# Kernel optimization log

Measured on AMD Instinct MI355X. Metric: run time of the kernel, lower is better.

## Reference

```python
import jax, jax.numpy as jnp
import numpy as np

B, T, V, D, L, FFM = 2, 2048, 50257, 1024, 8, 2


def setup_inputs() -> dict:
    key = jax.random.key(0)
    ks = jax.random.split(key, 10)
    s = 0.02
    return {
        "input_ids": jax.random.randint(ks[0], (B, T), 0, V),
        "embed": jax.random.normal(ks[1], (V, D), jnp.float32) * s,
        "norm1_w": jnp.ones((L, D), jnp.float32),
        "norm2_w": jnp.ones((L, D), jnp.float32),
        "a_diag": jax.random.uniform(ks[2], (L, D), jnp.float32, 0.5, 0.99),
        "W_in": jax.random.normal(ks[3], (L, D, D), jnp.float32) * s,
        "b_in": jnp.zeros((L, D), jnp.float32),
        "W_out": jax.random.normal(ks[4], (L, D, D), jnp.float32) * s,
        "ff_w1": jax.random.normal(ks[5], (L, D, FFM * D), jnp.float32) * s,
        "ff_b1": jnp.zeros((L, FFM * D), jnp.float32),
        "ff_w2": jax.random.normal(ks[6], (L, FFM * D, D), jnp.float32) * s,
        "ff_b2": jnp.zeros((L, D), jnp.float32),
        "final_norm_w": jnp.ones((D,), jnp.float32),
        "lm_head_w": jax.random.normal(ks[7], (V, D), jnp.float32) * s,
    }


def rmsnorm(x, w, eps=1e-6):
    return x * jax.lax.rsqrt(jnp.mean(x * x, axis=-1, keepdims=True) + eps) * w


def chaos_core(x, a, Win, bin_, Wout):
    pre = jnp.einsum('btd,de->bte', x, Win) + bin_  # precompute input drive (parallel)

    def step(s, p):
        s = jnp.tanh(a * s + p)
        return s, s

    s0 = jnp.zeros((x.shape[0], x.shape[-1]), x.dtype)
    _, hs = jax.lax.scan(step, s0, jnp.swapaxes(pre, 0, 1))  # (T, B, D)
    hs = jnp.swapaxes(hs, 0, 1)  # (B, T, D)
    return jnp.einsum('btd,de->bte', hs, Wout)


def reference(input_ids, embed, norm1_w, norm2_w, a_diag, W_in, b_in, W_out,
              ff_w1, ff_b1, ff_w2, ff_b2, final_norm_w, lm_head_w):
    x = embed[input_ids]  # (B, T, D)
    for i in range(L):
        # input_norm -> core -> residual
        x = x + chaos_core(rmsnorm(x, norm1_w[i]), a_diag[i], W_in[i], b_in[i], W_out[i])
        # ff_norm -> FeedForward (Linear -> SiLU -> Linear) -> residual
        h = rmsnorm(x, norm2_w[i])
        h = jax.nn.silu(jnp.einsum('btd,df->btf', h, ff_w1[i]) + ff_b1[i])
        x = x + jnp.einsum('btf,fd->btd', h, ff_w2[i]) + ff_b2[i]
    x = rmsnorm(x, final_norm_w)
    return jnp.einsum('btd,vd->btv', x, lm_head_w)  # logits (B, T, V)
```

## Files before the change

### kernel.cpp

```cpp
#include <hip/hip_runtime.h>

typedef unsigned short u16;
typedef __bf16 bf16x8 __attribute__((ext_vector_type(8)));
typedef float f32x4 __attribute__((ext_vector_type(4)));
typedef unsigned short u16x4 __attribute__((ext_vector_type(4)));

__device__ __forceinline__ u16 f2bf(float f) {
  union { float f; unsigned int u; } v; v.f = f;
  return (u16)((v.u + 0x7FFFu + ((v.u >> 16) & 1u)) >> 16);
}

__device__ __forceinline__ void gload16(const void* g, void* l) {
  __builtin_amdgcn_global_load_lds(
      (const __attribute__((address_space(1))) unsigned int*)g,
      (__attribute__((address_space(3))) unsigned int*)l, 16, 0, 0);
}

__global__ void transpose_cast_kernel(const float* __restrict__ W, u16* __restrict__ WT,
                                      int R, int C) {
  __shared__ float tile[32][33];
  const int tx = threadIdx.x, ty = threadIdx.y;
  const size_t zoff = (size_t)blockIdx.z * R * C;
  const int c0 = blockIdx.x * 32, r0 = blockIdx.y * 32;
#pragma unroll
  for (int k = 0; k < 32; k += 8)
    tile[ty + k][tx] = W[zoff + (size_t)(r0 + ty + k) * C + (c0 + tx)];
  __syncthreads();
#pragma unroll
  for (int k = 0; k < 32; k += 8)
    WT[zoff + (size_t)(c0 + ty + k) * R + (r0 + tx)] = f2bf(tile[tx][ty + k]);
}

__global__ void lm_cast_kernel(const float* __restrict__ lm, u16* __restrict__ out) {
  const int row = blockIdx.x;
  const int t = threadIdx.x;
  u16x4 o = {0, 0, 0, 0};
  if (row < 50257) {
    float4 v = *(const float4*)(lm + (size_t)row * 1024 + t * 4);
    o.x = f2bf(v.x); o.y = f2bf(v.y); o.z = f2bf(v.z); o.w = f2bf(v.w);
  }
  *(u16x4*)(out + (size_t)row * 1024 + t * 4) = o;
}

__global__ void embed_kernel(const int* __restrict__ ids, const float* __restrict__ embed,
                             float* __restrict__ x) {
  const int row = blockIdx.x;
  const int id = ids[row];
  const int t = threadIdx.x;
  *(float4*)(x + (size_t)row * 1024 + t * 4) =
      *(const float4*)(embed + (size_t)id * 1024 + t * 4);
}

__global__ void rmsnorm_kernel(const float* __restrict__ x, const float* __restrict__ w,
                               u16* __restrict__ out) {
  const int row = blockIdx.x, tid = threadIdx.x;
  const float* xr = x + (size_t)row * 1024;
  float4 v = *(const float4*)(xr + tid * 4);
  float ss = v.x * v.x + v.y * v.y + v.z * v.z + v.w * v.w;
#pragma unroll
  for (int off = 32; off; off >>= 1) ss += __shfl_xor(ss, off);
  __shared__ float red[4];
  if ((tid & 63) == 0) red[tid >> 6] = ss;
  __syncthreads();
  const float tot = red[0] + red[1] + red[2] + red[3];
  const float r = rsqrtf(tot * (1.0f / 1024.0f) + 1e-6f);
  float4 wv = *(const float4*)(w + tid * 4);
  u16x4 o;
  o.x = f2bf(v.x * r * wv.x); o.y = f2bf(v.y * r * wv.y);
  o.z = f2bf(v.z * r * wv.z); o.w = f2bf(v.w * r * wv.w);
  *(u16x4*)(out + (size_t)row * 1024 + tid * 4) = o;
}

__device__ __forceinline__ void sload(const float* __restrict__ p, int tb,
                                      float A2b, float (&buf)[8]) {
#pragma unroll
  for (int j = 0; j < 8; j++)
    buf[j] = fmaf(p[(size_t)(tb + j) * 1024], 2.8853900817779268f, A2b);
}

__device__ __forceinline__ void scomp(float (&buf)[8], float m2A2, float& r,
                                      u16* __restrict__ o, int tb) {
#pragma unroll
  for (int j = 0; j < 8; j++) {
    float z = fmaf(m2A2, r, buf[j]);
    float e = __builtin_amdgcn_exp2f(z);
    r = __builtin_amdgcn_rcpf(1.0f + e);
    o[(size_t)(tb + j) * 1024] = f2bf(fmaf(-2.0f, r, 1.0f));
  }
}

__global__ __launch_bounds__(256) void scan_kernel(const float* __restrict__ pre,
                                                   const float* __restrict__ a_diag,
                                                   const float* __restrict__ b_in,
                                                   u16* __restrict__ hs) {
  const int T = 2048;
  const int idx = blockIdx.x * 256 + threadIdx.x;
  const int b = idx >> 10, d = idx & 1023;
  const float* p = pre + (size_t)b * T * 1024 + d;
  u16* o = hs + (size_t)b * T * 1024 + d;
  const float A2 = a_diag[d] * 2.8853900817779268f;
  const float A2b = fmaf(2.8853900817779268f, b_in[d], A2);
  const float m2A2 = -2.0f * A2;
  float r = 0.5f;
  float b0[8], b1[8], b2[8], b3[8];
  sload(p, 0, A2b, b0); sload(p, 8, A2b, b1);
  sload(p, 16, A2b, b2); sload(p, 24, A2b, b3);
  for (int t0 = 0; t0 < T; t0 += 32) {
    scomp(b0, m2A2, r, o, t0);
    if (t0 + 32 < T) sload(p, t0 + 32, A2b, b0);
    scomp(b1, m2A2, r, o, t0 + 8);
    if (t0 + 32 < T) sload(p, t0 + 40, A2b, b1);
    scomp(b2, m2A2, r, o, t0 + 16);
    if (t0 + 32 < T) sload(p, t0 + 48, A2b, b2);
    scomp(b3, m2A2, r, o, t0 + 24);
    if (t0 + 32 < T) sload(p, t0 + 56, A2b, b3);
  }
}

template <int EPI>
__global__ __launch_bounds__(256) void gemmL(
    const u16* __restrict__ A, int lda, const u16* __restrict__ Bw, int ldb,
    const float* __restrict__ bias, float* Cf, u16* __restrict__ Cb,
    int ldc, int K) {
  __shared__ char lds[49152];
  const int tid = threadIdx.x;
  const int lane = tid & 63;
  const int wc = tid >> 6;
  const int tm = blockIdx.y * 64, tn = blockIdx.x * 128;
  const int lr = lane & 15;
  const int sb0 = ((lane >> 4) ^ (lane & 7)) << 4;

  const int srow = tid >> 3;
  const int sxs = ((tid & 7) ^ (srow & 7)) << 4;
  const char* pA = (const char*)A + (size_t)(tm + srow) * lda * 2 + sxs;
  const char* pB = (const char*)Bw + (size_t)(tn + srow) * ldb * 2 + sxs;
  const size_t a32 = (size_t)lda * 64;
  const size_t b32 = (size_t)ldb * 64;

#define STGL(kt, bufo)                                \
  {                                                   \
    char* d = lds + (bufo) + tid * 16;                \
    const size_t kb = (size_t)(kt) << 7;              \
    gload16(pA + kb, d);                              \
    gload16(pA + a32 + kb, d + 4096);                 \
    gload16(pB + kb, d + 8192);                       \
    gload16(pB + b32 + kb, d + 12288);                \
    gload16(pB + 2 * b32 + kb, d + 16384);            \
    gload16(pB + 3 * b32 + kb, d + 20480);            \
  }

  f32x4 acc[4][2] = {};
  const int nkt = K >> 6;

  STGL(0, 0);
  int cur = 0;
  for (int kt = 0; kt < nkt; ++kt) {
    if (kt + 1 < nkt) {
      STGL(kt + 1, (cur ^ 1) * 24576);
      asm volatile("s_waitcnt vmcnt(6)" ::: "memory");
    } else {
      asm volatile("s_waitcnt vmcnt(0)" ::: "memory");
    }
    __builtin_amdgcn_s_barrier();
    const char* base = lds + cur * 24576;
    bf16x8 aF[4][2], bF[2][2];
#pragma unroll
    for (int m = 0; m < 4; m++)
#pragma unroll
      for (int ks = 0; ks < 2; ks++)
        aF[m][ks] =
            *(const bf16x8*)(base + (m * 16 + lr) * 128 + (sb0 ^ (ks << 6)));
#pragma unroll
    for (int n = 0; n < 2; n++)
#pragma unroll
      for (int ks = 0; ks < 2; ks++)
        bF[n][ks] = *(const bf16x8*)(base + 8192 +
                                     (wc * 32 + n * 16 + lr) * 128 +
                                     (sb0 ^ (ks << 6)));
#pragma unroll
    for (int ks = 0; ks < 2; ks++)
#pragma unroll
      for (int m = 0; m < 4; m++)
#pragma unroll
        for (int n = 0; n < 2; n++)
          acc[m][n] = __builtin_amdgcn_mfma_f32_16x16x32_bf16(
              aF[m][ks], bF[n][ks], acc[m][n], 0, 0, 0);
    __builtin_amdgcn_s_barrier();
    cur ^= 1;
  }
#undef STGL

  const int crow = tm + ((lane >> 4) << 2);
  const int ccol = tn + wc * 32 + lr;
#pragma unroll
  for (int m = 0; m < 4; m++) {
#pragma unroll
    for (int n = 0; n < 2; n++) {
      const int cg = ccol + n * 16;
      float bb = 0.0f;
      if (EPI == 2 || EPI == 3) bb = bias[cg];
#pragma unroll
      for (int j = 0; j < 4; j++) {
        const size_t off = (size_t)(crow + m * 16 + j) * ldc + cg;
        const float v = acc[m][n][j] + bb;
        if (EPI == 0) {
          Cf[off] = v;
        } else if (EPI == 1) {
          Cf[off] += v;
        } else if (EPI == 2) {
          const float sg = __builtin_amdgcn_rcpf(
              1.0f + __builtin_amdgcn_exp2f(-1.4426950408889634f * v));
          Cb[off] = f2bf(v * sg);
        } else {
          Cf[off] += v;
        }
      }
    }
  }
}

__global__ __launch_bounds__(512, 2) void gemm_lm8(
    const u16* __restrict__ A, const u16* __restrict__ Bw,
    float* __restrict__ C, int Nreal) {
  __shared__ char lds[131072];
  const int tid = threadIdx.x;
  const int lane = tid & 63;
  const int wid = tid >> 6;
  const int wr = wid >> 2;
  const int wc = wid & 3;
  const int bid = blockIdx.x;
  const int tm = (((bid & 7) << 1) + ((bid >> 3) & 1)) << 8;
  const int tn = (bid >> 4) << 8;

  const int srow = tid >> 3;
  const int sxor = ((tid & 7) ^ (srow & 7)) << 4;
  const char* pAs = (const char*)A + ((size_t)(tm + srow) << 11) + sxor;
  const char* pBs = (const char*)Bw + ((size_t)(tn + srow) << 11) + sxor;

#define STG(p, h, kt, ro)                                      \
  {                                                            \
    char* d = lds + (ro) + tid * 16;                           \
    const char* s = (p) + ((size_t)(h) << 18) + ((kt) << 7);   \
    gload16(s, d);                                             \
    gload16(s + (64ull << 11), d + 8192);                      \
  }

  const int lr = lane & 15;
  const int sb0 = (((lane >> 4) ^ (lane & 7)) << 4);
  const int sb[2] = {sb0, sb0 ^ 64};
  const int aB = wr * 16384 + lr * 128;
  const int bB = 32768 + (wc >> 1) * 16384 + ((wc & 1) * 64 + lr) * 128;

  bf16x8 aR[4][2], bR[2][2][2];
  f32x4 acc[8][4] = {};

#define LDA_Q(bufo, mq)                                                         \
  _Pragma("unroll") for (int m_ = 0; m_ < 4; m_++)                              \
  _Pragma("unroll") for (int k_ = 0; k_ < 2; k_++)                              \
      aR[m_][k_] = *(const bf16x8*)(lds + (bufo) + aB + (mq)*8192 + m_*2048 + sb[k_]);

#define LDB_Q(bufo, nq)                                                         \
  _Pragma("unroll") for (int n_ = 0; n_ < 2; n_++)                              \
  _Pragma("unroll") for (int k_ = 0; k_ < 2; k_++)                              \
      bR[nq][n_][k_] = *(const bf16x8*)(lds + (bufo) + bB + (nq)*4096 + n_*2048 + sb[k_]);

#define MFMA_Q(mq, nq)                                                          \
  __builtin_amdgcn_s_setprio(1);                                                \
  _Pragma("unroll") for (int m_ = 0; m_ < 4; m_++)                              \
  _Pragma("unroll") for (int n_ = 0; n_ < 2; n_++)                              \
  _Pragma("unroll") for (int k_ = 0; k_ < 2; k_++)                              \
      acc[(mq)*4 + m_][(nq)*2 + n_] = __builtin_amdgcn_mfma_f32_16x16x32_bf16(  \
          aR[m_][k_], bR[nq][n_][k_], acc[(mq)*4 + m_][(nq)*2 + n_], 0, 0, 0);  \
  __builtin_amdgcn_s_setprio(0);

#define BAR() __builtin_amdgcn_s_barrier()
#define LGKM0() asm volatile("s_waitcnt lgkmcnt(0)" ::: "memory")

  STG(pAs, 0, 0, 0);
  STG(pAs, 1, 0, 16384);
  STG(pBs, 0, 0, 32768);
  STG(pBs, 1, 0, 49152);
  STG(pBs, 0, 1, 65536 + 32768);
  STG(pBs, 1, 1, 65536 + 49152);
  asm volatile("s_waitcnt vmcnt(4)" ::: "memory");
  BAR();

  for (int it = 0; it < 8; ++it) {
    const int t1 = 2 * it + 1, t2 = 2 * it + 2, t3 = 2 * it + 3;
    const bool st = (it < 7);
    LDA_Q(0, 0); LDB_Q(0, 0);
    STG(pAs, 0, t1, 65536);
    BAR(); LGKM0(); MFMA_Q(0, 0); BAR();
    LDB_Q(0, 1);
    STG(pAs, 1, t1, 65536 + 16384);
    BAR(); LGKM0(); MFMA_Q(0, 1); BAR();
    LDA_Q(0, 1);
    if (st) STG(pBs, 0, t2, 32768);
    BAR(); LGKM0(); MFMA_Q(1, 0); BAR();
    if (st) STG(pBs, 1, t2, 49152);
    BAR(); LGKM0(); MFMA_Q(1, 1);
    if (st) { asm volatile("s_waitcnt vmcnt(4)" ::: "memory"); }
    else    { asm volatile("s_waitcnt vmcnt(0)" ::: "memory"); }
    BAR();
    LDA_Q(65536, 0); LDB_Q(65536, 0);
    if (st) STG(pAs, 0, t2, 0);
    BAR(); LGKM0(); MFMA_Q(0, 0); BAR();
    LDB_Q(65536, 1);
    if (st) STG(pAs, 1, t2, 16384);
    BAR(); LGKM0(); MFMA_Q(0, 1); BAR();
    LDA_Q(65536, 1);
    if (st) STG(pBs, 0, t3, 65536 + 32768);
    BAR(); LGKM0(); MFMA_Q(1, 0); BAR();
    if (st) STG(pBs, 1, t3, 65536 + 49152);
    BAR(); LGKM0(); MFMA_Q(1, 1);
    if (st) { asm volatile("s_waitcnt vmcnt(4)" ::: "memory"); }
    else    { asm volatile("s_waitcnt vmcnt(0)" ::: "memory"); }
    BAR();
  }
#undef STG
#undef LDA_Q
#undef LDB_Q
#undef MFMA_Q
#undef BAR
#undef LGKM0

  const int crow = tm + wr * 128 + ((lane >> 4) << 2);
  const int ccol = tn + wc * 64 + lr;
#pragma unroll
  for (int M_ = 0; M_ < 8; M_++) {
    const int r = crow + (M_ >> 2) * 64 + (M_ & 3) * 16;
#pragma unroll
    for (int N_ = 0; N_ < 4; N_++) {
      const int cg = ccol + (N_ >> 1) * 32 + (N_ & 1) * 16;
      if (cg < Nreal) {
#pragma unroll
        for (int j = 0; j < 4; j++)
          __builtin_nontemporal_store(acc[M_][N_][j],
                                      &C[(size_t)(r + j) * Nreal + cg]);
      }
    }
  }
}

extern "C" void kernel_launch(void* const* d_in, const int* in_sizes, int n_in,
                              void* d_out, int out_size, void* d_ws, size_t ws_size,
                              hipStream_t stream) {
  const int D = 1024, V = 50257, L = 8;
  const int M = 4096;
  const int Vpad = 50432;
  const size_t MD = (size_t)M * D;

  const int* ids = (const int*)d_in[0];
  const float* embedw = (const float*)d_in[1];
  const float* norm1_w = (const float*)d_in[2];
  const float* norm2_w = (const float*)d_in[3];
  const float* a_diag = (const float*)d_in[4];
  const float* W_in = (const float*)d_in[5];
  const float* b_in = (const float*)d_in[6];
  const float* W_out = (const float*)d_in[7];
  const float* ff_w1 = (const float*)d_in[8];
  const float* ff_b1 = (const float*)d_in[9];
  const float* ff_w2 = (const float*)d_in[10];
  const float* ff_b2 = (const float*)d_in[11];
  const float* final_norm_w = (const float*)d_in[12];
  const float* lm_head_w = (const float*)d_in[13];

  char* w = (char*)d_ws;
  float* x = (float*)w;   w += MD * 4;
  u16* h = (u16*)w;       w += MD * 2;
  float* pre = (float*)w; w += MD * 4;
  u16* hs = (u16*)w;      w += MD * 2;
  u16* hff = (u16*)w;     w += MD * 2 * 2;
  u16* WinT = (u16*)w;    w += (size_t)L * D * D * 2;
  u16* WoutT = (u16*)w;   w += (size_t)L * D * D * 2;
  u16* ffw1T = (u16*)w;   w += (size_t)L * 2 * D * D * 2;
  u16* ffw2T = (u16*)w;   w += (size_t)L * 2 * D * D * 2;
  u16* lmpad = (u16*)w;   w += (size_t)Vpad * D * 2;

  lm_cast_kernel<<<Vpad, 256, 0, stream>>>(lm_head_w, lmpad);
  transpose_cast_kernel<<<dim3(32, 32, L), dim3(32, 8), 0, stream>>>(W_in, WinT, D, D);
  transpose_cast_kernel<<<dim3(64, 32, L), dim3(32, 8), 0, stream>>>(ff_w1, ffw1T, D, 2 * D);
  transpose_cast_kernel<<<dim3(32, 32, L), dim3(32, 8), 0, stream>>>(W_out, WoutT, D, D);
  transpose_cast_kernel<<<dim3(32, 64, L), dim3(32, 8), 0, stream>>>(ff_w2, ffw2T, 2 * D, D);

  embed_kernel<<<M, 256, 0, stream>>>(ids, embedw, x);

  for (int l = 0; l < L; l++) {
    rmsnorm_kernel<<<M, 256, 0, stream>>>(x, norm1_w + (size_t)l * D, h);
    gemmL<0><<<dim3(8, 64), 256, 0, stream>>>(
        h, D, WinT + (size_t)l * D * D, D, nullptr, pre, nullptr, D, D);
    scan_kernel<<<8, 256, 0, stream>>>(pre, a_diag + (size_t)l * D,
                                       b_in + (size_t)l * D, hs);
    gemmL<1><<<dim3(8, 64), 256, 0, stream>>>(
        hs, D, WoutT + (size_t)l * D * D, D, nullptr, x, nullptr, D, D);
    rmsnorm_kernel<<<M, 256, 0, stream>>>(x, norm2_w + (size_t)l * D, h);
    gemmL<2><<<dim3(16, 64), 256, 0, stream>>>(
        h, D, ffw1T + (size_t)l * 2 * D * D, D, ff_b1 + (size_t)l * 2 * D,
        nullptr, hff, 2 * D, D);
    gemmL<3><<<dim3(8, 64), 256, 0, stream>>>(
        hff, 2 * D, ffw2T + (size_t)l * 2 * D * D, 2 * D,
        ff_b2 + (size_t)l * D, x, nullptr, D, 2 * D);
  }

  rmsnorm_kernel<<<M, 256, 0, stream>>>(x, final_norm_w, h);
  gemm_lm8<<<dim3(8 * 394), 512, 0, stream>>>(h, lmpad, (float*)d_out, V);
}
```

Baseline: 3.027 ms.

## Fuse RMSNorm into GEMM prologue and fold norm weights into transposed weights

```diff
diff --git a/kernel.cpp b/kernel.cpp
--- a/kernel.cpp
+++ b/kernel.cpp
@@ -4,6 +4,7 @@
 typedef __bf16 bf16x8 __attribute__((ext_vector_type(8)));
 typedef float f32x4 __attribute__((ext_vector_type(4)));
 typedef unsigned short u16x4 __attribute__((ext_vector_type(4)));
+typedef unsigned short u16x8 __attribute__((ext_vector_type(8)));
 
 __device__ __forceinline__ u16 f2bf(float f) {
   union { float f; unsigned int u; } v; v.f = f;
@@ -16,19 +17,47 @@
       (__attribute__((address_space(3))) unsigned int*)l, 16, 0, 0);
 }
 
-__global__ void transpose_cast_kernel(const float* __restrict__ W, u16* __restrict__ WT,
-                                      int R, int C) {
+__global__ void prep_weights(const float* __restrict__ Win,
+                             const float* __restrict__ Wout,
+                             const float* __restrict__ ffw1,
+                             const float* __restrict__ ffw2,
+                             const float* __restrict__ n1w,
+                             const float* __restrict__ n2w,
+                             u16* __restrict__ WinT, u16* __restrict__ WoutT,
+                             u16* __restrict__ f1T, u16* __restrict__ f2T) {
   __shared__ float tile[32][33];
+  const int tk = blockIdx.x;
+  const float* src; u16* dst; const float* wm = nullptr;
+  int R, C, tr, tc;
+  if (tk < 8192) {
+    const int l = tk >> 10, rem = tk & 1023;
+    R = 1024; C = 1024; tr = rem >> 5; tc = rem & 31;
+    src = Win + (size_t)l * 1048576; dst = WinT + (size_t)l * 1048576;
+    wm = n1w + l * 1024;
+  } else if (tk < 16384) {
+    const int q = tk - 8192, l = q >> 10, rem = q & 1023;
+    R = 1024; C = 1024; tr = rem >> 5; tc = rem & 31;
+    src = Wout + (size_t)l * 1048576; dst = WoutT + (size_t)l * 1048576;
+  } else if (tk < 32768) {
+    const int q = tk - 16384, l = q >> 11, rem = q & 2047;
+    R = 1024; C = 2048; tr = rem >> 6; tc = rem & 63;
+    src = ffw1 + (size_t)l * 2097152; dst = f1T + (size_t)l * 2097152;
+    wm = n2w + l * 1024;
+  } else {
+    const int q = tk - 32768, l = q >> 11, rem = q & 2047;
+    R = 2048; C = 1024; tr = rem >> 5; tc = rem & 31;
+    src = ffw2 + (size_t)l * 2097152; dst = f2T + (size_t)l * 2097152;
+  }
   const int tx = threadIdx.x, ty = threadIdx.y;
-  const size_t zoff = (size_t)blockIdx.z * R * C;
-  const int c0 = blockIdx.x * 32, r0 = blockIdx.y * 32;
+  const int c0 = tc * 32, r0 = tr * 32;
 #pragma unroll
   for (int k = 0; k < 32; k += 8)
-    tile[ty + k][tx] = W[zoff + (size_t)(r0 + ty + k) * C + (c0 + tx)];
+    tile[ty + k][tx] = src[(size_t)(r0 + ty + k) * C + (c0 + tx)];
   __syncthreads();
+  const float wv = wm ? wm[r0 + tx] : 1.0f;
 #pragma unroll
   for (int k = 0; k < 32; k += 8)
-    WT[zoff + (size_t)(c0 + ty + k) * R + (r0 + tx)] = f2bf(tile[tx][ty + k]);
+    dst[(size_t)(c0 + ty + k) * R + (r0 + tx)] = f2bf(tile[tx][ty + k] * wv);
 }
 
 __global__ void lm_cast_kernel(const float* __restrict__ lm, u16* __restrict__ out) {
@@ -120,8 +149,7 @@
 template <int EPI>
 __global__ __launch_bounds__(256) void gemmL(
     const u16* __restrict__ A, int lda, const u16* __restrict__ Bw, int ldb,
-    const float* __restrict__ bias, float* Cf, u16* __restrict__ Cb,
-    int ldc, int K) {
+    const float* __restrict__ bias, float* Cf, int ldc, int K) {
   __shared__ char lds[49152];
   const int tid = threadIdx.x;
   const int lane = tid & 63;
@@ -197,22 +225,149 @@
 #pragma unroll
     for (int n = 0; n < 2; n++) {
       const int cg = ccol + n * 16;
-      float bb = 0.0f;
-      if (EPI == 2 || EPI == 3) bb = bias[cg];
+      const float bb = (EPI == 3) ? bias[cg] : 0.0f;
+#pragma unroll
+      for (int j = 0; j < 4; j++) {
+        const size_t off = (size_t)(crow + m * 16 + j) * ldc + cg;
+        Cf[off] += acc[m][n][j] + bb;
+      }
+    }
+  }
+}
+
+template <int EPI>
+__global__ __launch_bounds__(256) void gemmLF(
+    const float* __restrict__ X, const u16* __restrict__ Bw, int ldb,
+    const float* __restrict__ bias, float* __restrict__ Cf,
+    u16* __restrict__ Cb, int ldc) {
+  __shared__ char lds[50432];
+  float* red = (float*)(lds + 49152);
+  float* rinvs = (float*)(lds + 50176);
+  const int tid = threadIdx.x;
+  const int lane = tid & 63;
+  const int wc = tid >> 6;
+  const int tm = blockIdx.y * 64, tn = blockIdx.x * 128;
+  const int lr = lane & 15;
+  const int sb0 = ((lane >> 4) ^ (lane & 7)) << 4;
+
+  {
+    const float* xr = X + (size_t)(tm + (tid >> 2)) * 1024 + (tid & 3) * 256;
+    float ss = 0.f;
+#pragma unroll 8
+    for (int j = 0; j < 64; j++) {
+      float4 v = *(const float4*)(xr + j * 4);
+      ss += v.x * v.x + v.y * v.y + v.z * v.z + v.w * v.w;
+    }
+    red[tid] = ss;
+  }
+  __syncthreads();
+  if (tid < 64)
+    rinvs[tid] = rsqrtf((red[tid * 4] + red[tid * 4 + 1] + red[tid * 4 + 2] +
+                         red[tid * 4 + 3]) * (1.0f / 1024.0f) + 1e-6f);
+  __syncthreads();
+  const float rv = rinvs[tid >> 2];
+
+  const int srow = tid >> 3;
+  const int sxs = ((tid & 7) ^ (srow & 7)) << 4;
+  const char* pB = (const char*)Bw + (size_t)(tn + srow) * ldb * 2 + sxs;
+  const size_t b32 = (size_t)ldb * 64;
+  const int arow = tid >> 2;
+  const float* xa = X + (size_t)(tm + arow) * 1024 + (tid & 3) * 16;
+  char* const da = lds + arow * 128;
+  const int as0 = (((tid & 3) * 2) ^ (arow & 7)) << 4;
+  const int as1 = (((tid & 3) * 2 + 1) ^ (arow & 7)) << 4;
+
+#define STB(kt, bufo)                                            \
+  {                                                              \
+    char* d = lds + (bufo) + 8192 + tid * 16;                    \
+    const size_t kb = (size_t)(kt) << 7;                         \
+    gload16(pB + kb, d);                                         \
+    gload16(pB + b32 + kb, d + 4096);                            \
+    gload16(pB + 2 * b32 + kb, d + 8192);                        \
+    gload16(pB + 3 * b32 + kb, d + 12288);                       \
+  }
+#define CVT8(o_, v0_, v1_)                                       \
+  o_[0] = f2bf(v0_.x * rv); o_[1] = f2bf(v0_.y * rv);            \
+  o_[2] = f2bf(v0_.z * rv); o_[3] = f2bf(v0_.w * rv);            \
+  o_[4] = f2bf(v1_.x * rv); o_[5] = f2bf(v1_.y * rv);            \
+  o_[6] = f2bf(v1_.z * rv); o_[7] = f2bf(v1_.w * rv);
+
+  f32x4 acc[4][2] = {};
+
+  {
+    const float* s0 = xa;
+    float4 v0 = *(const float4*)(s0), v1 = *(const float4*)(s0 + 4);
+    float4 v2 = *(const float4*)(s0 + 8), v3 = *(const float4*)(s0 + 12);
+    u16x8 o0, o1;
+    CVT8(o0, v0, v1); CVT8(o1, v2, v3);
+    *(u16x8*)(da + as0) = o0; *(u16x8*)(da + as1) = o1;
+    STB(0, 0);
+  }
+  __syncthreads();
+
+  int cur = 0;
+  for (int kt = 0; kt < 16; ++kt) {
+    const int nb = (cur ^ 1) * 24576;
+    float4 v0, v1, v2, v3;
+    if (kt < 15) {
+      const float* s_ = xa + (kt + 1) * 64;
+      v0 = *(const float4*)(s_); v1 = *(const float4*)(s_ + 4);
+      v2 = *(const float4*)(s_ + 8); v3 = *(const float4*)(s_ + 12);
+      STB(kt + 1, nb);
+    }
+    const char* base = lds + cur * 24576;
+    bf16x8 aF[4][2], bF[2][2];
+#pragma unroll
+    for (int m = 0; m < 4; m++)
+#pragma unroll
+      for (int ks = 0; ks < 2; ks++)
+        aF[m][ks] =
+            *(const bf16x8*)(base + (m * 16 + lr) * 128 + (sb0 ^ (ks << 6)));
+#pragma unroll
+    for (int n = 0; n < 2; n++)
+#pragma unroll
+      for (int ks = 0; ks < 2; ks++)
+        bF[n][ks] = *(const bf16x8*)(base + 8192 +
+                                     (wc * 32 + n * 16 + lr) * 128 +
+                                     (sb0 ^ (ks << 6)));
+#pragma unroll
+    for (int ks = 0; ks < 2; ks++)
+#pragma unroll
+      for (int m = 0; m < 4; m++)
+#pragma unroll
+        for (int n = 0; n < 2; n++)
+          acc[m][n] = __builtin_amdgcn_mfma_f32_16x16x32_bf16(
+              aF[m][ks], bF[n][ks], acc[m][n], 0, 0, 0);
+    if (kt < 15) {
+      u16x8 o0, o1;
+      CVT8(o0, v0, v1); CVT8(o1, v2, v3);
+      *(u16x8*)(lds + nb + (da - lds) + as0) = o0;
+      *(u16x8*)(lds + nb + (da - lds) + as1) = o1;
+    }
+    __syncthreads();
+    cur ^= 1;
+  }
+#undef STB
+#undef CVT8
+
+  const int crow = tm + ((lane >> 4) << 2);
+  const int ccol = tn + wc * 32 + lr;
+#pragma unroll
+  for (int m = 0; m < 4; m++) {
+#pragma unroll
+    for (int n = 0; n < 2; n++) {
+      const int cg = ccol + n * 16;
+      const float bb = (EPI == 2) ? bias[cg] : 0.0f;
 #pragma unroll
       for (int j = 0; j < 4; j++) {
         const size_t off = (size_t)(crow + m * 16 + j) * ldc + cg;
         const float v = acc[m][n][j] + bb;
         if (EPI == 0) {
           Cf[off] = v;
-        } else if (EPI == 1) {
-          Cf[off] += v;
-        } else if (EPI == 2) {
+        } else {
           const float sg = __builtin_amdgcn_rcpf(
               1.0f + __builtin_amdgcn_exp2f(-1.4426950408889634f * v));
           Cb[off] = f2bf(v * sg);
-        } else {
-          Cf[off] += v;
         }
       }
     }
@@ -335,8 +490,7 @@
       if (cg < Nreal) {
 #pragma unroll
         for (int j = 0; j < 4; j++)
-          __builtin_nontemporal_store(acc[M_][N_][j],
-                                      &C[(size_t)(r + j) * Nreal + cg]);
+          C[(size_t)(r + j) * Nreal + cg] = acc[M_][N_][j];
       }
     }
   }
@@ -377,29 +531,24 @@
   u16* ffw2T = (u16*)w;   w += (size_t)L * 2 * D * D * 2;
   u16* lmpad = (u16*)w;   w += (size_t)Vpad * D * 2;
 
+  prep_weights<<<49152, dim3(32, 8), 0, stream>>>(
+      W_in, W_out, ff_w1, ff_w2, norm1_w, norm2_w, WinT, WoutT, ffw1T, ffw2T);
   lm_cast_kernel<<<Vpad, 256, 0, stream>>>(lm_head_w, lmpad);
-  transpose_cast_kernel<<<dim3(32, 32, L), dim3(32, 8), 0, stream>>>(W_in, WinT, D, D);
-  transpose_cast_kernel<<<dim3(64, 32, L), dim3(32, 8), 0, stream>>>(ff_w1, ffw1T, D, 2 * D);
-  transpose_cast_kernel<<<dim3(32, 32, L), dim3(32, 8), 0, stream>>>(W_out, WoutT, D, D);
-  transpose_cast_kernel<<<dim3(32, 64, L), dim3(32, 8), 0, stream>>>(ff_w2, ffw2T, 2 * D, D);
-
   embed_kernel<<<M, 256, 0, stream>>>(ids, embedw, x);
 
   for (int l = 0; l < L; l++) {
-    rmsnorm_kernel<<<M, 256, 0, stream>>>(x, norm1_w + (size_t)l * D, h);
-    gemmL<0><<<dim3(8, 64), 256, 0, stream>>>(
-        h, D, WinT + (size_t)l * D * D, D, nullptr, pre, nullptr, D, D);
+    gemmLF<0><<<dim3(8, 64), 256, 0, stream>>>(
+        x, WinT + (size_t)l * D * D, D, nullptr, pre, nullptr, D);
     scan_kernel<<<8, 256, 0, stream>>>(pre, a_diag + (size_t)l * D,
                                        b_in + (size_t)l * D, hs);
     gemmL<1><<<dim3(8, 64), 256, 0, stream>>>(
-        hs, D, WoutT + (size_t)l * D * D, D, nullptr, x, nullptr, D, D);
-    rmsnorm_kernel<<<M, 256, 0, stream>>>(x, norm2_w + (size_t)l * D, h);
-    gemmL<2><<<dim3(16, 64), 256, 0, stream>>>(
-        h, D, ffw1T + (size_t)l * 2 * D * D, D, ff_b1 + (size_t)l * 2 * D,
-        nullptr, hff, 2 * D, D);
+        hs, D, WoutT + (size_t)l * D * D, D, nullptr, x, D, D);
+    gemmLF<2><<<dim3(16, 64), 256, 0, stream>>>(
+        x, ffw1T + (size_t)l * 2 * D * D, D, ff_b1 + (size_t)l * 2 * D,
+        nullptr, hff, 2 * D);
     gemmL<3><<<dim3(8, 64), 256, 0, stream>>>(
         hff, 2 * D, ffw2T + (size_t)l * 2 * D * D, 2 * D,
-        ff_b2 + (size_t)l * D, x, nullptr, D, 2 * D);
+        ff_b2 + (size_t)l * D, x, D, 2 * D);
   }
 
   rmsnorm_kernel<<<M, 256, 0, stream>>>(x, final_norm_w, h);
```

After: 3.183 ms. 5.1% more time.
